# Optimization experiments

Measured on AMD Instinct MI355X. Metric: run time of the kernel, lower is better.

The kernel has to match this reference:

```python
import jax, jax.numpy as jnp
import numpy as np

B, M, N, T = 16, 16, 32, 80


def setup_inputs() -> dict:
    key = jax.random.key(0)
    ks = jax.random.split(key, 20)
    p = lambda k, shp: jax.random.normal(k, shp, jnp.float32) * 0.05
    return {
        "ego_traj": jax.random.normal(ks[0], (B, M, T, 6), jnp.float32),
        "ego_encoding": jax.random.normal(ks[1], (B, 256), jnp.float32),
        "agents_traj": jax.random.normal(ks[2], (B, M, N, T, 3), jnp.float32),
        "agents_states": jax.random.normal(ks[3], (B, N, 11), jnp.float32),
        # interaction_feature_encoder: Linear(10,64) -> ReLU -> Linear(64,256)
        "enc_w1": p(ks[4], (10, 64)), "enc_b1": p(ks[5], (64,)),
        "enc_w2": p(ks[6], (64, 256)), "enc_b2": p(ks[7], (256,)),
        # interaction_feature_decoder: Linear(256,64) -> ELU -> Linear(64,4) -> Sigmoid
        "dec_w1": p(ks[8], (256, 64)), "dec_b1": p(ks[9], (64,)),
        "dec_w2": p(ks[10], (64, 4)), "dec_b2": p(ks[11], (4,)),
        # weights_decoder: Linear(256,64) -> ELU -> Linear(64,8) -> Softplus
        "wd_w1": p(ks[12], (256, 64)), "wd_b1": p(ks[13], (64,)),
        "wd_w2": p(ks[14], (64, 8)), "wd_b2": p(ks[15], (8,)),
        "timesteps": 80,
    }


def reference(ego_traj, ego_encoding, agents_traj, agents_states,
              enc_w1, enc_b1, enc_w2, enc_b2,
              dec_w1, dec_b1, dec_w2, dec_b2,
              wd_w1, wd_b1, wd_w2, wd_b2, timesteps):
    Tm = timesteps
    # ---- hardcoded ego features: B,M,4 ----
    speed = ego_traj[:, :, :Tm, 3]
    acc = ego_traj[:, :, :Tm, 4]
    jerk = jnp.diff(acc, axis=-1) / 0.1
    jerk = jnp.concatenate([jerk[:, :, :1], jerk], axis=-1)
    curvature = ego_traj[:, :, :Tm, 5]
    lat_acc = speed ** 2 * curvature
    hard = jnp.stack([
        -jnp.clip(speed.mean(-1), 0.0, 15.0) / 15.0,
        jnp.clip(jnp.abs(acc).mean(-1), 0.0, 4.0) / 4.0,
        jnp.clip(jnp.abs(jerk).mean(-1), 0.0, 6.0) / 6.0,
        jnp.clip(jnp.abs(lat_acc).mean(-1), 0.0, 5.0) / 5.0,
    ], axis=-1)  # B,M,4

    # ---- latent interaction features (vectorized over M) ----
    agent_mask = (agents_states.sum(-1) != 0).astype(ego_traj.dtype)  # B,N
    ry = agents_traj[:, :, :, :Tm, 2] - ego_traj[:, :, None, :Tm, 2]  # B,M,N,T
    ry = jnp.arctan2(jnp.sin(ry), jnp.cos(ry))
    rp = agents_traj[:, :, :, :Tm, :2] - ego_traj[:, :, None, :Tm, :2]
    rp = jnp.stack([rp[..., 0] * jnp.cos(ry), rp[..., 1] * jnp.sin(ry)], axis=-1)
    av = jnp.diff(agents_traj[:, :, :, :Tm, :2], axis=-2) / 0.1
    av = jnp.concatenate([av[:, :, :, :1, :], av], axis=-2)
    evx = ego_traj[:, :, :Tm, 3] * jnp.cos(ego_traj[:, :, :Tm, 2])  # B,M,T
    evy = ego_traj[:, :, :Tm, 3] * jnp.sin(ego_traj[:, :, :Tm, 2])
    rv = jnp.stack([(av[..., 0] - evx[:, :, None]) * jnp.cos(ry),
                    (av[..., 1] - evy[:, :, None]) * jnp.sin(ry)], axis=-1)
    rel = jnp.concatenate([rp, ry[..., None], rv], axis=-1)  # B,M,N,T,5
    aattr = jnp.broadcast_to(agents_states[:, None, :, None, 6:], rel.shape[:4] + (5,))
    attr = jnp.concatenate([rel, aattr], axis=-1) * agent_mask[:, None, :, None, None]  # B,M,N,T,10
    h = jax.nn.relu(attr @ enc_w1 + enc_b1) @ enc_w2 + enc_b2  # B,M,N,T,256
    feat = h.max(axis=2).mean(axis=2)  # max over agents, mean over time -> B,M,256
    inter = jax.nn.sigmoid(jax.nn.elu(feat @ dec_w1 + dec_b1) @ dec_w2 + dec_b2)  # B,M,4

    # ---- weights (variable_cost=False -> ones_like encoding) ----
    enc_in = jnp.ones_like(ego_encoding)
    weights = jax.nn.softplus(jax.nn.elu(enc_in @ wd_w1 + wd_b1) @ wd_w2 + wd_b2)  # B,8

    # ---- collision cost: B,M ----
    dist = jnp.linalg.norm(ego_traj[:, :, None, :Tm, :2] - agents_traj[:, :, :, :Tm, :2], axis=-1)
    coll = (jnp.exp(-0.2 * dist ** 2) * agent_mask[:, None, :, None]).sum((-1, -2))

    feats = jnp.concatenate([hard, inter], axis=-1)  # B,M,8
    scores = -jnp.sum(feats * weights[:, None, :], axis=-1) - 10.0 * coll
    ego_mask = ego_traj.sum(-1).sum(-1) != 0  # B,M
    scores = jnp.where(ego_mask, scores, -jnp.inf)
    return scores, weights
```

## Files before the change

kernel.cpp:

```cpp
#include <hip/hip_runtime.h>
#include <hip/hip_bf16.h>
#include <math.h>

typedef __attribute__((ext_vector_type(8))) short bf16x8;
typedef __attribute__((ext_vector_type(4))) float f32x4;

#define NB 16
#define NM 16
#define NN 32
#define NT 80
#define TC 10
#define NP 8

#define WS_WTS 0
#define WS_BF 16
#define WS_BTBL 8208
#define WS_BASE 40976
#define WS_BM_STRIDE 2112
#define WS_SC_OFF 2048

__device__ __forceinline__ unsigned pk2bf(float lo, float hi) {
  __hip_bfloat162 h = __float22bfloat162_rn(make_float2(lo, hi));
  return *reinterpret_cast<unsigned*>(&h);
}
__device__ __forceinline__ short f2bf(float f) {
  unsigned u = __float_as_uint(f);
  u += 0x7fffu + ((u >> 16) & 1u);
  return (short)(u >> 16);
}

__global__ void prep_kernel(const float* __restrict__ agents_states,
                            const float* __restrict__ enc_w1,
                            const float* __restrict__ enc_b1,
                            const float* __restrict__ enc_w2,
                            const float* __restrict__ wd_w1,
                            const float* __restrict__ wd_b1,
                            const float* __restrict__ wd_w2,
                            const float* __restrict__ wd_b2,
                            float* __restrict__ ws,
                            float* __restrict__ out) {
  const int blk = blockIdx.x;
  const int tid = threadIdx.x;
  if (blk < NB) {
    __shared__ float smask[NN];
    if (tid < NN) {
      const float* st = agents_states + ((size_t)blk * NN + tid) * 11;
      float s = 0.f;
      for (int i = 0; i < 11; ++i) s += st[i];
      smask[tid] = (s != 0.f) ? 1.f : 0.f;
    }
    __syncthreads();
    for (int e = tid; e < NN * 64; e += 256) {
      int n = e >> 6, j = e & 63;
      const float* st = agents_states + ((size_t)blk * NN + n) * 11 + 6;
      float acc = st[0] * enc_w1[5 * 64 + j] + st[1] * enc_w1[6 * 64 + j] +
                  st[2] * enc_w1[7 * 64 + j] + st[3] * enc_w1[8 * 64 + j] +
                  st[4] * enc_w1[9 * 64 + j];
      ws[WS_BTBL + blk * (NN * 64) + e] = smask[n] * acc + enc_b1[j];
    }
  } else {
    __shared__ float sh[64];
    if (tid < 64) {
      float acc = wd_b1[tid];
      for (int i = 0; i < 256; ++i) acc += wd_w1[i * 64 + tid];
      sh[tid] = acc > 0.f ? acc : expm1f(acc);
    }
    __syncthreads();
    if (tid < 8) {
      float acc = wd_b2[tid];
      for (int k = 0; k < 64; ++k) acc += sh[k] * wd_w2[k * 8 + tid];
      float sp = log1pf(__expf(acc));
      ws[WS_WTS + tid] = sp;
      for (int b = 0; b < NB; ++b) out[NB * NM + b * 8 + tid] = sp;
    }
    const int g = tid >> 6;
    const int lane = tid & 63;
    bf16x8* bft = reinterpret_cast<bf16x8*>(ws + WS_BF);
#pragma unroll
    for (int q = 0; q < 8; ++q) {
      int s = g * 8 + q;
      int wv = s >> 3, ct = (s >> 1) & 3, kt = s & 1;
      int col = wv * 64 + ct * 16 + (lane & 15);
      int krow = (lane >> 4) * 8;
      bf16x8 v;
#pragma unroll
      for (int j = 0; j < 8; ++j)
        v[j] = f2bf(enc_w2[(kt * 32 + krow + j) * 256 + col]);
      bft[s * 64 + lane] = v;
    }
  }
}

__global__ __launch_bounds__(256, 4) void score_partial(
    const float* __restrict__ ego_traj,
    const float* __restrict__ agents_traj,
    const float* __restrict__ agents_states,
    const float* __restrict__ enc_w1,
    float* __restrict__ ws)
{
  __shared__ float s_rel[5][TC][NN + 1];
  __shared__ __align__(16) short s_hidden[2][NN * 64];
  __shared__ float s_ego[TC][5];
  __shared__ float s_acc[TC + 2];
  __shared__ float s_spd[TC], s_lat[TC], s_egos[TC];
  __shared__ float s_mask[NN];
  __shared__ float s_collpart[256];
  __shared__ float s_cw[32];

  const int bid = blockIdx.x;
  const int bm = bid >> 3;
  const int p = bid & 7;
  const int t0 = p * TC;
  const int b = bm >> 4;
  const int tid = threadIdx.x;
  const int lane = tid & 63;
  const int wv = tid >> 6;

  float* ws_bm = ws + WS_BASE + (size_t)bm * WS_BM_STRIDE;

  if (tid < TC) {
    int i = tid;
    const float* e = ego_traj + ((size_t)bm * NT + (t0 + i)) * 6;
    float ex = e[0], ey = e[1], eh = e[2], spd = e[3], acc = e[4], cur = e[5];
    s_ego[i][0] = ex; s_ego[i][1] = ey; s_ego[i][2] = eh;
    s_ego[i][3] = spd * __cosf(eh);
    s_ego[i][4] = spd * __sinf(eh);
    s_spd[i] = spd;
    s_acc[i + 1] = acc;
    s_lat[i] = fabsf(spd * spd * cur);
    s_egos[i] = ex + ey + eh + spd + acc + cur;
  } else if (tid == TC) {
    int tp = (p == 0) ? 0 : (t0 - 1);
    s_acc[0] = ego_traj[((size_t)bm * NT + tp) * 6 + 4];
  } else if (tid >= 64 && tid < 64 + NN) {
    int n = tid - 64;
    const float* st = agents_states + ((size_t)b * NN + n) * 11;
    float s = 0.f;
    for (int i = 0; i < 11; ++i) s += st[i];
    s_mask[n] = (s != 0.f) ? 1.f : 0.f;
  }

  const int jq = tid & 15;
  const int nh = tid >> 4;
  const int na = nh, nb_ = nh + 16;
  const int j0 = jq * 4;

  float w1r[5][4];
#pragma unroll
  for (int i = 0; i < 5; ++i)
#pragma unroll
    for (int jj = 0; jj < 4; ++jj)
      w1r[i][jj] = enc_w1[i * 64 + j0 + jj];

  bf16x8 Bf[4][2];
  {
    const bf16x8* bft = reinterpret_cast<const bf16x8*>(ws + WS_BF);
#pragma unroll
    for (int ct = 0; ct < 4; ++ct)
#pragma unroll
      for (int kt = 0; kt < 2; ++kt) {
        int s = ((wv * 4 + ct) * 2 + kt);
        Bf[ct][kt] = bft[s * 64 + lane];
      }
  }

  float baseA[4], baseBB[4];
  {
    const f32x4* bt = reinterpret_cast<const f32x4*>(ws + WS_BTBL + b * (NN * 64));
    f32x4 fa = bt[na * 16 + jq];
    f32x4 fb = bt[nb_ * 16 + jq];
#pragma unroll
    for (int jj = 0; jj < 4; ++jj) { baseA[jj] = fa[jj]; baseBB[jj] = fb[jj]; }
  }
  __syncthreads();

  {
    float collacc = 0.f;
    const float* atraj = agents_traj + (size_t)bm * (NN * NT * 3);
#pragma unroll
    for (int k = 0; k < 2; ++k) {
      int pp = tid + k * 256;
      if (pp < NN * TC) {
        int n = pp / TC;
        int i = pp - n * TC;
        int tg = t0 + i;
        const float* bp = atraj + n * (NT * 3) + tg * 3;
        float ax = bp[0], ay = bp[1], ah = bp[2];
        float avx, avy;
        if (tg == 0) { avx = (bp[3] - ax) * 10.f; avy = (bp[4] - ay) * 10.f; }
        else         { avx = (ax - bp[-3]) * 10.f; avy = (ay - bp[-2]) * 10.f; }
        float ex = s_ego[i][0], ey = s_ego[i][1], eh = s_ego[i][2];
        float evx = s_ego[i][3], evy = s_ego[i][4];
        float m = s_mask[n];
        float ryr = ah - eh;
        float w = ryr - 6.283185307179586f * rintf(ryr * 0.15915494309189535f);
        float cy = __cosf(ryr), sy = __sinf(ryr);
        float dx = ax - ex, dy = ay - ey;
        s_rel[0][i][n] = dx * cy * m;
        s_rel[1][i][n] = dy * sy * m;
        s_rel[2][i][n] = w * m;
        s_rel[3][i][n] = (avx - evx) * cy * m;
        s_rel[4][i][n] = (avy - evy) * sy * m;
        collacc += __expf(-0.2f * (dx * dx + dy * dy)) * m;
      }
    }
    s_collpart[tid] = collacc;
  }

  if (tid >= 251) {
    int which = tid - 251;
    float s = 0.f;
    if (which == 0)      { for (int i = 0; i < TC; ++i) s += s_spd[i]; }
    else if (which == 1) { for (int i = 0; i < TC; ++i) s += fabsf(s_acc[i + 1]); }
    else if (which == 2) {
      for (int i = 0; i < TC; ++i) {
        int ia = (p == 0 && i == 0) ? 2 : (i + 1);
        s += fabsf((s_acc[ia] - s_acc[ia - 1]) * 10.f);
      }
    }
    else if (which == 3) { for (int i = 0; i < TC; ++i) s += s_lat[i]; }
    else                 { for (int i = 0; i < TC; ++i) s += s_egos[i]; }
    ws_bm[WS_SC_OFF + p * 8 + which] = s;
  }

  const int wbyteA = (na * 128 + jq * 8) ^ ((na & 7) << 4);
  const int wbyteB = (nb_ * 128 + jq * 8) ^ ((nb_ & 7) << 4);
  int abyte[2][2];
  {
    int nbl = lane & 15;
    int kb = (lane >> 4) * 16;
#pragma unroll
    for (int rt = 0; rt < 2; ++rt) {
      int row = rt * 16 + nbl;
#pragma unroll
      for (int kt = 0; kt < 2; ++kt)
        abyte[rt][kt] = (row * 128 + kt * 64 + kb) ^ ((row & 7) << 4);
    }
  }

  auto compute_hidden = [&](int i, int buf) {
    float r0a = s_rel[0][i][na], r1a = s_rel[1][i][na], r2a = s_rel[2][i][na],
          r3a = s_rel[3][i][na], r4a = s_rel[4][i][na];
    float r0b = s_rel[0][i][nb_], r1b = s_rel[1][i][nb_], r2b = s_rel[2][i][nb_],
          r3b = s_rel[3][i][nb_], r4b = s_rel[4][i][nb_];
    float pa[4], pb[4];
#pragma unroll
    for (int jj = 0; jj < 4; ++jj) {
      pa[jj] = fmaxf(baseA[jj] + r0a * w1r[0][jj] + r1a * w1r[1][jj] +
                     r2a * w1r[2][jj] + r3a * w1r[3][jj] + r4a * w1r[4][jj], 0.f);
      pb[jj] = fmaxf(baseBB[jj] + r0b * w1r[0][jj] + r1b * w1r[1][jj] +
                     r2b * w1r[2][jj] + r3b * w1r[3][jj] + r4b * w1r[4][jj], 0.f);
    }
    char* hb = reinterpret_cast<char*>(&s_hidden[buf][0]);
    uint2 ua = {pk2bf(pa[0], pa[1]), pk2bf(pa[2], pa[3])};
    uint2 ub = {pk2bf(pb[0], pb[1]), pk2bf(pb[2], pb[3])};
    *reinterpret_cast<uint2*>(hb + wbyteA) = ua;
    *reinterpret_cast<uint2*>(hb + wbyteB) = ub;
  };

  float macc[4] = {0.f, 0.f, 0.f, 0.f};

  auto mfma_step = [&](int buf) {
    const char* hb = reinterpret_cast<const char*>(&s_hidden[buf][0]);
    bf16x8 a00 = *reinterpret_cast<const bf16x8*>(hb + abyte[0][0]);
    bf16x8 a01 = *reinterpret_cast<const bf16x8*>(hb + abyte[0][1]);
    bf16x8 a10 = *reinterpret_cast<const bf16x8*>(hb + abyte[1][0]);
    bf16x8 a11 = *reinterpret_cast<const bf16x8*>(hb + abyte[1][1]);
#pragma unroll
    for (int ct = 0; ct < 4; ++ct) {
      f32x4 c0 = {0.f, 0.f, 0.f, 0.f}, c1 = {0.f, 0.f, 0.f, 0.f};
      c0 = __builtin_amdgcn_mfma_f32_16x16x32_bf16(a00, Bf[ct][0], c0, 0, 0, 0);
      c0 = __builtin_amdgcn_mfma_f32_16x16x32_bf16(a01, Bf[ct][1], c0, 0, 0, 0);
      c1 = __builtin_amdgcn_mfma_f32_16x16x32_bf16(a10, Bf[ct][0], c1, 0, 0, 0);
      c1 = __builtin_amdgcn_mfma_f32_16x16x32_bf16(a11, Bf[ct][1], c1, 0, 0, 0);
      float v = fmaxf(fmaxf(fmaxf(c0[0], c1[0]), fmaxf(c0[1], c1[1])),
                      fmaxf(fmaxf(c0[2], c1[2]), fmaxf(c0[3], c1[3])));
      v = fmaxf(v, __shfl_xor(v, 16));
      v = fmaxf(v, __shfl_xor(v, 32));
      macc[ct] += v;
    }
  };

  __syncthreads();
  compute_hidden(0, 0);
  __syncthreads();

  for (int i = 0; i < TC; ++i) {
    const int buf = i & 1;
    if (i + 1 < TC) compute_hidden(i + 1, buf ^ 1);
    mfma_step(buf);
    __syncthreads();
  }

  if (lane < 16) {
#pragma unroll
    for (int ct = 0; ct < 4; ++ct)
      ws_bm[p * 256 + wv * 64 + ct * 16 + lane] = macc[ct];
  }
  if (tid < 32) {
    float s = 0.f;
#pragma unroll
    for (int k = 0; k < 8; ++k) s += s_collpart[tid + k * 32];
    s_cw[tid] = s;
  }
  __syncthreads();
  if (tid == 0) {
    float c = 0.f;
    for (int i = 0; i < 32; ++i) c += s_cw[i];
    ws_bm[WS_SC_OFF + p * 8 + 5] = c;
  }
}

__global__ void combine_kernel(const float* __restrict__ ws,
                               const float* __restrict__ enc_b2,
                               const float* __restrict__ dec_w1,
                               const float* __restrict__ dec_b1,
                               const float* __restrict__ dec_w2,
                               const float* __restrict__ dec_b2,
                               float* __restrict__ out_scores) {
  __shared__ float s_feat[256];
  __shared__ float s_dh[64];
  __shared__ float s_hard[4];
  __shared__ float s_inter[4];
  __shared__ float s_mc[2];
  const int bm = blockIdx.x;
  const int tid = threadIdx.x;
  const float* wb = ws + WS_BASE + (size_t)bm * WS_BM_STRIDE;

  for (int c = tid; c < 256; c += 64) {
    float f = 0.f;
#pragma unroll
    for (int pp = 0; pp < NP; ++pp) f += wb[pp * 256 + c];
    s_feat[c] = f * (1.f / NT) + enc_b2[c];
  }
  const float* sc = wb + WS_SC_OFF;
  if (tid < 6) {
    float s = 0.f;
#pragma unroll
    for (int pp = 0; pp < NP; ++pp) s += sc[pp * 8 + tid];
    if (tid == 0) s_hard[0] = -fminf(fmaxf(s * (1.f / NT), 0.f), 15.f) * (1.f / 15.f);
    if (tid == 1) s_hard[1] = fminf(fmaxf(s * (1.f / NT), 0.f), 4.f) * 0.25f;
    if (tid == 2) s_hard[2] = fminf(fmaxf(s * (1.f / NT), 0.f), 6.f) * (1.f / 6.f);
    if (tid == 3) s_hard[3] = fminf(fmaxf(s * (1.f / NT), 0.f), 5.f) * 0.2f;
    if (tid == 4) s_mc[0] = s;
    if (tid == 5) s_mc[1] = s;
  }
  __syncthreads();

  {
    float a0 = 0.f, a1 = 0.f, a2 = 0.f, a3 = 0.f;
    for (int i = 0; i < 256; i += 4) {
      a0 += s_feat[i + 0] * dec_w1[(i + 0) * 64 + tid];
      a1 += s_feat[i + 1] * dec_w1[(i + 1) * 64 + tid];
      a2 += s_feat[i + 2] * dec_w1[(i + 2) * 64 + tid];
      a3 += s_feat[i + 3] * dec_w1[(i + 3) * 64 + tid];
    }
    float acc = dec_b1[tid] + ((a0 + a1) + (a2 + a3));
    s_dh[tid] = acc > 0.f ? acc : expm1f(acc);
  }
  __syncthreads();

  if (tid < 4) {
    float acc = dec_b2[tid];
    for (int k = 0; k < 64; ++k) acc += s_dh[k] * dec_w2[k * 4 + tid];
    s_inter[tid] = 1.f / (1.f + __expf(-acc));
  }
  __syncthreads();

  if (tid == 0) {
    const float* wts = ws + WS_WTS;
    float scv = 0.f;
#pragma unroll
    for (int i = 0; i < 4; ++i) scv += s_hard[i] * wts[i];
#pragma unroll
    for (int i = 0; i < 4; ++i) scv += s_inter[i] * wts[4 + i];
    scv = -scv - 10.f * s_mc[1];
    if (s_mc[0] == 0.f) scv = -INFINITY;
    out_scores[bm] = scv;
  }
}

extern "C" void kernel_launch(void* const* d_in, const int* in_sizes, int n_in,
                              void* d_out, int out_size, void* d_ws, size_t ws_size,
                              hipStream_t stream) {
  const float* ego_traj      = (const float*)d_in[0];
  const float* agents_traj   = (const float*)d_in[2];
  const float* agents_states = (const float*)d_in[3];
  const float* enc_w1 = (const float*)d_in[4];
  const float* enc_b1 = (const float*)d_in[5];
  const float* enc_w2 = (const float*)d_in[6];
  const float* enc_b2 = (const float*)d_in[7];
  const float* dec_w1 = (const float*)d_in[8];
  const float* dec_b1 = (const float*)d_in[9];
  const float* dec_w2 = (const float*)d_in[10];
  const float* dec_b2 = (const float*)d_in[11];
  const float* wd_w1 = (const float*)d_in[12];
  const float* wd_b1 = (const float*)d_in[13];
  const float* wd_w2 = (const float*)d_in[14];
  const float* wd_b2 = (const float*)d_in[15];

  float* out = (float*)d_out;
  float* ws = (float*)d_ws;

  prep_kernel<<<NB + 1, 256, 0, stream>>>(agents_states, enc_w1, enc_b1, enc_w2,
                                          wd_w1, wd_b1, wd_w2, wd_b2, ws, out);
  score_partial<<<NB * NM * NP, 256, 0, stream>>>(
      ego_traj, agents_traj, agents_states, enc_w1, ws);
  combine_kernel<<<NB * NM, 64, 0, stream>>>(
      ws, enc_b2, dec_w1, dec_b1, dec_w2, dec_b2, out);
}
```

Measured before the change: 49.23 us.

## Switch hidden layer to packed fp16 math and fp16 MFMA, wave-reduce collision sum

Measured after the change: 45.96 us. 6.6% less time.

```diff
diff --git a/kernel.cpp b/kernel.cpp
--- a/kernel.cpp
+++ b/kernel.cpp
@@ -1,8 +1,11 @@
 #include <hip/hip_runtime.h>
-#include <hip/hip_bf16.h>
+#include <hip/hip_fp16.h>
 #include <math.h>
-
-typedef __attribute__((ext_vector_type(8))) short bf16x8;
+#include <string.h>
+
+typedef __attribute__((ext_vector_type(8))) short short8;
+typedef __attribute__((ext_vector_type(8))) _Float16 f16x8;
+typedef __attribute__((ext_vector_type(2))) _Float16 h2;
 typedef __attribute__((ext_vector_type(4))) float f32x4;
 
 #define NB 16
@@ -14,19 +17,17 @@
 
 #define WS_WTS 0
 #define WS_BF 16
-#define WS_BTBL 8208
-#define WS_BASE 40976
+#define WS_BB 8208
+#define WS_BASE 24592
 #define WS_BM_STRIDE 2112
 #define WS_SC_OFF 2048
 
-__device__ __forceinline__ unsigned pk2bf(float lo, float hi) {
-  __hip_bfloat162 h = __float22bfloat162_rn(make_float2(lo, hi));
-  return *reinterpret_cast<unsigned*>(&h);
-}
-__device__ __forceinline__ short f2bf(float f) {
-  unsigned u = __float_as_uint(f);
-  u += 0x7fffu + ((u >> 16) & 1u);
-  return (short)(u >> 16);
+__device__ __forceinline__ short f2h(float f) {
+  _Float16 h = (_Float16)f;
+  short s; memcpy(&s, &h, 2); return s;
+}
+__device__ __forceinline__ unsigned h2bits(h2 h) {
+  unsigned u; memcpy(&u, &h, 4); return u;
 }
 
 __global__ void prep_kernel(const float* __restrict__ agents_states,
@@ -50,13 +51,21 @@
       smask[tid] = (s != 0.f) ? 1.f : 0.f;
     }
     __syncthreads();
-    for (int e = tid; e < NN * 64; e += 256) {
-      int n = e >> 6, j = e & 63;
+    h2* bb = reinterpret_cast<h2*>(ws + WS_BB) + blk * (NN * 32);
+    for (int e = tid; e < NN * 32; e += 256) {
+      int n = e >> 5, jp = e & 31;
       const float* st = agents_states + ((size_t)blk * NN + n) * 11 + 6;
-      float acc = st[0] * enc_w1[5 * 64 + j] + st[1] * enc_w1[6 * 64 + j] +
-                  st[2] * enc_w1[7 * 64 + j] + st[3] * enc_w1[8 * 64 + j] +
-                  st[4] * enc_w1[9 * 64 + j];
-      ws[WS_BTBL + blk * (NN * 64) + e] = smask[n] * acc + enc_b1[j];
+      float v[2];
+#pragma unroll
+      for (int hh = 0; hh < 2; ++hh) {
+        int j = jp * 2 + hh;
+        float acc = st[0] * enc_w1[5 * 64 + j] + st[1] * enc_w1[6 * 64 + j] +
+                    st[2] * enc_w1[7 * 64 + j] + st[3] * enc_w1[8 * 64 + j] +
+                    st[4] * enc_w1[9 * 64 + j];
+        v[hh] = smask[n] * acc + enc_b1[j];
+      }
+      h2 r; r[0] = (_Float16)v[0]; r[1] = (_Float16)v[1];
+      bb[e] = r;
     }
   } else {
     __shared__ float sh[64];
@@ -75,17 +84,17 @@
     }
     const int g = tid >> 6;
     const int lane = tid & 63;
-    bf16x8* bft = reinterpret_cast<bf16x8*>(ws + WS_BF);
+    short8* bft = reinterpret_cast<short8*>(ws + WS_BF);
 #pragma unroll
     for (int q = 0; q < 8; ++q) {
       int s = g * 8 + q;
       int wv = s >> 3, ct = (s >> 1) & 3, kt = s & 1;
       int col = wv * 64 + ct * 16 + (lane & 15);
       int krow = (lane >> 4) * 8;
-      bf16x8 v;
+      short8 v;
 #pragma unroll
       for (int j = 0; j < 8; ++j)
-        v[j] = f2bf(enc_w2[(kt * 32 + krow + j) * 256 + col]);
+        v[j] = f2h(enc_w2[(kt * 32 + krow + j) * 256 + col]);
       bft[s * 64 + lane] = v;
     }
   }
@@ -98,14 +107,13 @@
     const float* __restrict__ enc_w1,
     float* __restrict__ ws)
 {
-  __shared__ float s_rel[5][TC][NN + 1];
+  __shared__ h2 s_rel[5][TC][NN + 1];
   __shared__ __align__(16) short s_hidden[2][NN * 64];
   __shared__ float s_ego[TC][5];
   __shared__ float s_acc[TC + 2];
   __shared__ float s_spd[TC], s_lat[TC], s_egos[TC];
   __shared__ float s_mask[NN];
-  __shared__ float s_collpart[256];
-  __shared__ float s_cw[32];
+  __shared__ float s_cw[4];
 
   const int bid = blockIdx.x;
   const int bm = bid >> 3;
@@ -145,32 +153,34 @@
   const int na = nh, nb_ = nh + 16;
   const int j0 = jq * 4;
 
-  float w1r[5][4];
-#pragma unroll
-  for (int i = 0; i < 5; ++i)
-#pragma unroll
-    for (int jj = 0; jj < 4; ++jj)
-      w1r[i][jj] = enc_w1[i * 64 + j0 + jj];
-
-  bf16x8 Bf[4][2];
+  f16x8 Bf[4][2];
   {
-    const bf16x8* bft = reinterpret_cast<const bf16x8*>(ws + WS_BF);
+    const f16x8* bft = reinterpret_cast<const f16x8*>(ws + WS_BF);
 #pragma unroll
     for (int ct = 0; ct < 4; ++ct)
 #pragma unroll
-      for (int kt = 0; kt < 2; ++kt) {
-        int s = ((wv * 4 + ct) * 2 + kt);
-        Bf[ct][kt] = bft[s * 64 + lane];
-      }
-  }
-
-  float baseA[4], baseBB[4];
+      for (int kt = 0; kt < 2; ++kt)
+        Bf[ct][kt] = bft[((wv * 4 + ct) * 2 + kt) * 64 + lane];
+  }
+
+  h2 w1h[5][2];
+#pragma unroll
+  for (int f = 0; f < 5; ++f)
+#pragma unroll
+    for (int jp = 0; jp < 2; ++jp) {
+      h2 r;
+      r[0] = (_Float16)enc_w1[f * 64 + j0 + jp * 2];
+      r[1] = (_Float16)enc_w1[f * 64 + j0 + jp * 2 + 1];
+      w1h[f][jp] = r;
+    }
+
+  h2 baseA2[2], baseB2[2];
   {
-    const f32x4* bt = reinterpret_cast<const f32x4*>(ws + WS_BTBL + b * (NN * 64));
-    f32x4 fa = bt[na * 16 + jq];
-    f32x4 fb = bt[nb_ * 16 + jq];
-#pragma unroll
-    for (int jj = 0; jj < 4; ++jj) { baseA[jj] = fa[jj]; baseBB[jj] = fb[jj]; }
+    const h2* bb = reinterpret_cast<const h2*>(ws + WS_BB) + b * (NN * 32);
+    baseA2[0] = bb[na * 32 + jq * 2];
+    baseA2[1] = bb[na * 32 + jq * 2 + 1];
+    baseB2[0] = bb[nb_ * 32 + jq * 2];
+    baseB2[1] = bb[nb_ * 32 + jq * 2 + 1];
   }
   __syncthreads();
 
@@ -196,15 +206,25 @@
         float w = ryr - 6.283185307179586f * rintf(ryr * 0.15915494309189535f);
         float cy = __cosf(ryr), sy = __sinf(ryr);
         float dx = ax - ex, dy = ay - ey;
-        s_rel[0][i][n] = dx * cy * m;
-        s_rel[1][i][n] = dy * sy * m;
-        s_rel[2][i][n] = w * m;
-        s_rel[3][i][n] = (avx - evx) * cy * m;
-        s_rel[4][i][n] = (avy - evy) * sy * m;
+        float r0 = dx * cy * m, r1 = dy * sy * m, r2 = w * m;
+        float r3 = (avx - evx) * cy * m, r4 = (avy - evy) * sy * m;
+        h2 v0, v1, v2, v3, v4;
+        v0[0] = v0[1] = (_Float16)r0;
+        v1[0] = v1[1] = (_Float16)r1;
+        v2[0] = v2[1] = (_Float16)r2;
+        v3[0] = v3[1] = (_Float16)r3;
+        v4[0] = v4[1] = (_Float16)r4;
+        s_rel[0][i][n] = v0;
+        s_rel[1][i][n] = v1;
+        s_rel[2][i][n] = v2;
+        s_rel[3][i][n] = v3;
+        s_rel[4][i][n] = v4;
         collacc += __expf(-0.2f * (dx * dx + dy * dy)) * m;
       }
     }
-    s_collpart[tid] = collacc;
+#pragma unroll
+    for (int off = 1; off < 64; off <<= 1) collacc += __shfl_xor(collacc, off);
+    if (lane == 0) s_cw[wv] = collacc;
   }
 
   if (tid >= 251) {
@@ -238,22 +258,34 @@
     }
   }
 
+  h2 z2; z2[0] = z2[1] = (_Float16)0.f;
+
   auto compute_hidden = [&](int i, int buf) {
-    float r0a = s_rel[0][i][na], r1a = s_rel[1][i][na], r2a = s_rel[2][i][na],
-          r3a = s_rel[3][i][na], r4a = s_rel[4][i][na];
-    float r0b = s_rel[0][i][nb_], r1b = s_rel[1][i][nb_], r2b = s_rel[2][i][nb_],
-          r3b = s_rel[3][i][nb_], r4b = s_rel[4][i][nb_];
-    float pa[4], pb[4];
-#pragma unroll
-    for (int jj = 0; jj < 4; ++jj) {
-      pa[jj] = fmaxf(baseA[jj] + r0a * w1r[0][jj] + r1a * w1r[1][jj] +
-                     r2a * w1r[2][jj] + r3a * w1r[3][jj] + r4a * w1r[4][jj], 0.f);
-      pb[jj] = fmaxf(baseBB[jj] + r0b * w1r[0][jj] + r1b * w1r[1][jj] +
-                     r2b * w1r[2][jj] + r3b * w1r[3][jj] + r4b * w1r[4][jj], 0.f);
+    h2 ra0 = s_rel[0][i][na], ra1 = s_rel[1][i][na], ra2 = s_rel[2][i][na],
+       ra3 = s_rel[3][i][na], ra4 = s_rel[4][i][na];
+    h2 rb0 = s_rel[0][i][nb_], rb1 = s_rel[1][i][nb_], rb2 = s_rel[2][i][nb_],
+       rb3 = s_rel[3][i][nb_], rb4 = s_rel[4][i][nb_];
+    uint2 ua, ub;
+#pragma unroll
+    for (int jp = 0; jp < 2; ++jp) {
+      h2 ha = baseA2[jp];
+      ha = ra0 * w1h[0][jp] + ha;
+      ha = ra1 * w1h[1][jp] + ha;
+      ha = ra2 * w1h[2][jp] + ha;
+      ha = ra3 * w1h[3][jp] + ha;
+      ha = ra4 * w1h[4][jp] + ha;
+      ha = __builtin_elementwise_max(ha, z2);
+      h2 hb2 = baseB2[jp];
+      hb2 = rb0 * w1h[0][jp] + hb2;
+      hb2 = rb1 * w1h[1][jp] + hb2;
+      hb2 = rb2 * w1h[2][jp] + hb2;
+      hb2 = rb3 * w1h[3][jp] + hb2;
+      hb2 = rb4 * w1h[4][jp] + hb2;
+      hb2 = __builtin_elementwise_max(hb2, z2);
+      if (jp == 0) { ua.x = h2bits(ha); ub.x = h2bits(hb2); }
+      else         { ua.y = h2bits(ha); ub.y = h2bits(hb2); }
     }
     char* hb = reinterpret_cast<char*>(&s_hidden[buf][0]);
-    uint2 ua = {pk2bf(pa[0], pa[1]), pk2bf(pa[2], pa[3])};
-    uint2 ub = {pk2bf(pb[0], pb[1]), pk2bf(pb[2], pb[3])};
     *reinterpret_cast<uint2*>(hb + wbyteA) = ua;
     *reinterpret_cast<uint2*>(hb + wbyteB) = ub;
   };
@@ -262,17 +294,17 @@
 
   auto mfma_step = [&](int buf) {
     const char* hb = reinterpret_cast<const char*>(&s_hidden[buf][0]);
-    bf16x8 a00 = *reinterpret_cast<const bf16x8*>(hb + abyte[0][0]);
-    bf16x8 a01 = *reinterpret_cast<const bf16x8*>(hb + abyte[0][1]);
-    bf16x8 a10 = *reinterpret_cast<const bf16x8*>(hb + abyte[1][0]);
-    bf16x8 a11 = *reinterpret_cast<const bf16x8*>(hb + abyte[1][1]);
+    f16x8 a00 = *reinterpret_cast<const f16x8*>(hb + abyte[0][0]);
+    f16x8 a01 = *reinterpret_cast<const f16x8*>(hb + abyte[0][1]);
+    f16x8 a10 = *reinterpret_cast<const f16x8*>(hb + abyte[1][0]);
+    f16x8 a11 = *reinterpret_cast<const f16x8*>(hb + abyte[1][1]);
 #pragma unroll
     for (int ct = 0; ct < 4; ++ct) {
       f32x4 c0 = {0.f, 0.f, 0.f, 0.f}, c1 = {0.f, 0.f, 0.f, 0.f};
-      c0 = __builtin_amdgcn_mfma_f32_16x16x32_bf16(a00, Bf[ct][0], c0, 0, 0, 0);
-      c0 = __builtin_amdgcn_mfma_f32_16x16x32_bf16(a01, Bf[ct][1], c0, 0, 0, 0);
-      c1 = __builtin_amdgcn_mfma_f32_16x16x32_bf16(a10, Bf[ct][0], c1, 0, 0, 0);
-      c1 = __builtin_amdgcn_mfma_f32_16x16x32_bf16(a11, Bf[ct][1], c1, 0, 0, 0);
+      c0 = __builtin_amdgcn_mfma_f32_16x16x32_f16(a00, Bf[ct][0], c0, 0, 0, 0);
+      c0 = __builtin_amdgcn_mfma_f32_16x16x32_f16(a01, Bf[ct][1], c0, 0, 0, 0);
+      c1 = __builtin_amdgcn_mfma_f32_16x16x32_f16(a10, Bf[ct][0], c1, 0, 0, 0);
+      c1 = __builtin_amdgcn_mfma_f32_16x16x32_f16(a11, Bf[ct][1], c1, 0, 0, 0);
       float v = fmaxf(fmaxf(fmaxf(c0[0], c1[0]), fmaxf(c0[1], c1[1])),
                       fmaxf(fmaxf(c0[2], c1[2]), fmaxf(c0[3], c1[3])));
       v = fmaxf(v, __shfl_xor(v, 16));
@@ -297,18 +329,8 @@
     for (int ct = 0; ct < 4; ++ct)
       ws_bm[p * 256 + wv * 64 + ct * 16 + lane] = macc[ct];
   }
-  if (tid < 32) {
-    float s = 0.f;
-#pragma unroll
-    for (int k = 0; k < 8; ++k) s += s_collpart[tid + k * 32];
-    s_cw[tid] = s;
-  }
-  __syncthreads();
-  if (tid == 0) {
-    float c = 0.f;
-    for (int i = 0; i < 32; ++i) c += s_cw[i];
-    ws_bm[WS_SC_OFF + p * 8 + 5] = c;
-  }
+  if (tid == 0)
+    ws_bm[WS_SC_OFF + p * 8 + 5] = s_cw[0] + s_cw[1] + s_cw[2] + s_cw[3];
 }
 
 __global__ void combine_kernel(const float* __restrict__ ws,
```
